# Optimization experiments

Hardware: AMD Instinct MI355X
Metric: run time of the kernel (lower is better)

Reference implementation:

```python
import jax, jax.numpy as jnp
import numpy as np

B, T, C = 2, 1024, 1024
H = 16
HD = C // H
S = 512   # short_term_memory_size
L = 1024  # sum(long_term_memory_size)
THETA = 10000.0


def setup_inputs() -> dict:
    key = jax.random.key(0)
    ks = jax.random.split(key, 7)
    return {
        "x": jax.random.normal(ks[0], (B, T, C), jnp.float32),
        "short_term_memory": jax.random.normal(ks[1], (B, S, C), jnp.float32),
        "long_q": jax.random.normal(ks[2], (B, L, H, HD), jnp.float32),
        "long_k": jax.random.normal(ks[3], (B, L, H, HD), jnp.float32),
        "long_v": jax.random.normal(ks[4], (B, L, H, HD), jnp.float32),
        "w_attn": jax.random.normal(ks[5], (C, 3 * C), jnp.float32) * 0.02,
        "w_proj": jax.random.normal(ks[6], (C, C), jnp.float32) * 0.02,
    }


def _rope_cos_sin(seq_len, dim, theta):
    # llama-style precompute_freqs_cis: freqs over even indices, angles = t * freq
    inv = 1.0 / (theta ** (jnp.arange(0, dim, 2, dtype=jnp.float32) / dim))
    t = jnp.arange(seq_len, dtype=jnp.float32)
    ang = jnp.outer(t, inv)  # [seq, dim//2]
    return jnp.cos(ang), jnp.sin(ang)


def _apply_rope(x, cos, sin):
    # x: [B, seq, H, hd] viewed as interleaved complex pairs (llama apply_rotary_emb)
    xr = x.reshape(*x.shape[:-1], HD // 2, 2)
    x0, x1 = xr[..., 0], xr[..., 1]
    c = cos[None, :, None, :]
    s = sin[None, :, None, :]
    o0 = x0 * c - x1 * s
    o1 = x0 * s + x1 * c
    return jnp.stack([o0, o1], axis=-1).reshape(x.shape)


def _memory_mask():
    # create_memory_mask: tril over M=L+S+T, rows [L, L+S) fully visible
    M = L + S + T
    m = np.tril(np.ones((M, M), dtype=np.float32))
    m[L:L + S, :] = 1.0
    return jnp.asarray(m)


_MASK = _memory_mask()


def reference(x, short_term_memory, long_q, long_k, long_v, w_attn, w_proj):
    # prepend short-term memory tokens, project qkv
    xcat = jnp.concatenate([short_term_memory, x], axis=1)          # [B, S+T, C]
    qkv = xcat @ w_attn                                             # [B, S+T, 3C]
    q, k, v = jnp.split(qkv, 3, axis=-1)
    q = q.reshape(B, S + T, H, HD)
    k = k.reshape(B, S + T, H, HD)
    v = v.reshape(B, S + T, H, HD)
    # in-place rotary on the last S+T positions (long-term part untouched)
    cos, sin = _rope_cos_sin(S + T, HD, THETA)
    q = _apply_rope(q, cos, sin)
    k = _apply_rope(k, cos, sin)
    # concat pre-rotated long-term memory in front
    q = jnp.concatenate([long_q, q], axis=1)                        # [B, M, H, hd]
    k = jnp.concatenate([long_k, k], axis=1)
    v = jnp.concatenate([long_v, v], axis=1)
    q, k, v = (t.transpose(0, 2, 1, 3) for t in (q, k, v))          # [B, H, M, hd]
    att = jnp.einsum('bhqd,bhkd->bhqk', q, k) * (1.0 / jnp.sqrt(jnp.float32(HD)))
    att = jnp.where(_MASK == 0, -jnp.inf, att)
    att = jax.nn.softmax(att, axis=-1)
    y = jnp.einsum('bhqk,bhkd->bhqd', att, v)                       # [B, H, M, hd]
    y = y.transpose(0, 2, 1, 3).reshape(B, L + S + T, C)
    y = y[:, -T:, :] @ w_proj                                       # [B, T, C]
    return y
```

## Files before the change

kernel.cpp:

```cpp
#include <hip/hip_runtime.h>
#include <math.h>

#define BB 2
#define TT 1024
#define CC 1024
#define HH 16
#define HD 64
#define SS 512
#define LL 1024
#define ST 1536
#define MM 2560
#define C3 3072

typedef __attribute__((ext_vector_type(8))) short short8;
typedef __attribute__((ext_vector_type(4))) short short4v;
typedef __attribute__((ext_vector_type(4))) float floatx4;

__device__ __forceinline__ unsigned short f2bf(float f) {
    union { float f; unsigned u; } v; v.f = f;
    unsigned r = v.u + 0x7fffu + ((v.u >> 16) & 1u);
    return (unsigned short)(r >> 16);
}
__device__ __forceinline__ float bf2f(short s) {
    union { unsigned u; float f; } v;
    v.u = ((unsigned)(unsigned short)s) << 16;
    return v.f;
}

__device__ __forceinline__ void gl_lds16(const short* g, short* l) {
    __builtin_amdgcn_global_load_lds(
        (const __attribute__((address_space(1))) void*)g,
        (__attribute__((address_space(3))) void*)l,
        16, 0, 0);
}

__global__ __launch_bounds__(256)
void prep_all(const float* __restrict__ x, const float* __restrict__ stm,
              const float* __restrict__ w_attn, const float* __restrict__ w_proj,
              const float* __restrict__ lk, const float* __restrict__ lv,
              short* __restrict__ Xb, short* __restrict__ WaT,
              short* __restrict__ WpT, short* __restrict__ Kg,
              short* __restrict__ Vt, float* __restrict__ tab)
{
    __shared__ __align__(16) char smem[9216];
    const int blk = blockIdx.x;
    const int t = threadIdx.x;

    if (blk < 3072) {
        const int idx = blk * 256 + t;
        const int rg  = idx >> 8;
        const int c   = (idx & 255) << 2;
        const int b   = rg >= ST;
        const int r   = rg - b * ST;
        const float* src = (r < SS) ? (stm + ((size_t)b * SS + r) * CC + c)
                                    : (x   + ((size_t)b * TT + (r - SS)) * CC + c);
        float4 v = *(const float4*)src;
        short4v o;
        o.x = (short)f2bf(v.x); o.y = (short)f2bf(v.y);
        o.z = (short)f2bf(v.z); o.w = (short)f2bf(v.w);
        *(short4v*)(Xb + (size_t)rg * CC + c) = o;
    } else if (blk < 7168) {
        const bool isA = blk < 6144;
        const int bx = isA ? (blk - 3072) : (blk - 6144);
        const int nblk = isA ? 96 : 32;
        const int Nd = isA ? C3 : CC;
        const float* W = isA ? w_attn : w_proj;
        short* WT = isA ? WaT : WpT;
        const int n0 = (bx % nblk) * 32, k0 = (bx / nblk) * 32;
        float (*Tl)[33] = (float(*)[33])smem;
        const int r = t >> 3, c4 = (t & 7) << 2;
        float4 v = *(const float4*)(W + (size_t)(k0 + r) * Nd + n0 + c4);
        Tl[r][c4 + 0] = v.x; Tl[r][c4 + 1] = v.y;
        Tl[r][c4 + 2] = v.z; Tl[r][c4 + 3] = v.w;
        __syncthreads();
        short4v o;
        o.x = (short)f2bf(Tl[c4 + 0][r]); o.y = (short)f2bf(Tl[c4 + 1][r]);
        o.z = (short)f2bf(Tl[c4 + 2][r]); o.w = (short)f2bf(Tl[c4 + 3][r]);
        *(short4v*)(WT + (size_t)(n0 + r) * CC + k0 + c4) = o;
    } else if (blk < 7360) {
        const int idx = (blk - 7168) * 256 + t;
        const int r = idx >> 5, e = idx & 31;
        const float inv = powf(10000.0f, -(float)e * (1.0f / 32.0f));
        float sn, cs;
        sincosf((float)r * inv, &sn, &cs);
        tab[idx * 2] = cs;
        tab[idx * 2 + 1] = sn;
    } else {
        const int bx = blk - 7360;
        const int bh = bx >> 4, j0 = (bx & 15) * 64;
        const int b = bh >> 4, h = bh & 15;
        short (*Tl)[72] = (short(*)[72])smem;
        const int jr = t >> 2, c16 = (t & 3) << 4;
        const size_t si = (((size_t)b * LL + j0 + jr) * HH + h) * HD + c16;
        short kk[16], vv[16];
        #pragma unroll
        for (int u = 0; u < 4; u++) {
            float4 kv = *(const float4*)(lk + si + 4 * u);
            float4 vf = *(const float4*)(lv + si + 4 * u);
            kk[4*u+0] = (short)f2bf(kv.x); kk[4*u+1] = (short)f2bf(kv.y);
            kk[4*u+2] = (short)f2bf(kv.z); kk[4*u+3] = (short)f2bf(kv.w);
            vv[4*u+0] = (short)f2bf(vf.x); vv[4*u+1] = (short)f2bf(vf.y);
            vv[4*u+2] = (short)f2bf(vf.z); vv[4*u+3] = (short)f2bf(vf.w);
        }
        short* kdst = Kg + ((size_t)bh * MM + j0 + jr) * HD + c16;
        *(short8*)kdst       = *(short8*)&kk[0];
        *(short8*)(kdst + 8) = *(short8*)&kk[8];
        #pragma unroll
        for (int u = 0; u < 16; u++) Tl[jr][c16 + u] = vv[u];
        __syncthreads();
        const int r = t >> 2, c = t & 3;
        short o0[8], o1[8];
        #pragma unroll
        for (int u = 0; u < 8; u++) {
            o0[u] = Tl[c * 16 + u][r];
            o1[u] = Tl[c * 16 + 8 + u][r];
        }
        short* vdst = Vt + ((size_t)bh * HD + r) * MM + j0 + c * 16;
        *(short8*)vdst       = *(short8*)&o0[0];
        *(short8*)(vdst + 8) = *(short8*)&o1[0];
    }
}

__global__ __launch_bounds__(256)
void qkv_gemm(const short* __restrict__ A, const short* __restrict__ Bt,
              const float* __restrict__ RT,
              short* __restrict__ Qo, short* __restrict__ Ko, short* __restrict__ Vo)
{
    __shared__ short As[128 * 32];
    __shared__ short Bs[128 * 32];
    __shared__ short Et[128 * 132];
    const int b = blockIdx.z;
    const int row0 = blockIdx.y * 128, col0 = blockIdx.x * 128;
    const int tid = threadIdx.x;
    const int w = tid >> 6, l = tid & 63, quad = l >> 4, cl = l & 15;
    const int wr = w >> 1, wc = w & 1;

    const int reg  = col0 >> 10;
    const bool hasQ = (row0 >= SS);
    if (reg == 0 && !hasQ) return;

    const int srow = (l >> 2);
    const int schunk = ((l & 3) - (srow >> 1)) & 3;
    const int arow = w * 32 + srow;
    const short* gA0 = A + ((size_t)b * ST + row0 + arow) * CC + schunk * 8;
    const short* gA1 = gA0 + (size_t)16 * CC;
    const short* gB0 = Bt + (size_t)(col0 + arow) * CC + schunk * 8;
    const short* gB1 = gB0 + (size_t)16 * CC;
    short* lA0 = &As[(w * 32) * 32 + l * 8];
    short* lA1 = &As[(w * 32 + 16) * 32 + l * 8];
    short* lB0 = &Bs[(w * 32) * 32 + l * 8];
    short* lB1 = &Bs[(w * 32 + 16) * 32 + l * 8];

    const int fs = (quad + (cl >> 1)) & 3;

    floatx4 acc[4][4];
    #pragma unroll
    for (int mi = 0; mi < 4; mi++)
        #pragma unroll
        for (int ni = 0; ni < 4; ni++) acc[mi][ni] = (floatx4){0.f, 0.f, 0.f, 0.f};

    for (int k0 = 0; k0 < CC; k0 += 32) {
        __syncthreads();
        gl_lds16(gA0 + k0, lA0);
        gl_lds16(gA1 + k0, lA1);
        gl_lds16(gB0 + k0, lB0);
        gl_lds16(gB1 + k0, lB1);
        __syncthreads();
        short8 af[4], bf[4];
        #pragma unroll
        for (int mi = 0; mi < 4; mi++)
            af[mi] = *(const short8*)&As[(wr * 64 + mi * 16 + cl) * 32 + fs * 8];
        #pragma unroll
        for (int ni = 0; ni < 4; ni++)
            bf[ni] = *(const short8*)&Bs[(wc * 64 + ni * 16 + cl) * 32 + fs * 8];
        #pragma unroll
        for (int mi = 0; mi < 4; mi++)
            #pragma unroll
            for (int ni = 0; ni < 4; ni++)
                acc[mi][ni] = __builtin_amdgcn_mfma_f32_16x16x32_bf16(
                    af[mi], bf[ni], acc[mi][ni], 0, 0, 0);
    }

    #pragma unroll
    for (int ni = 0; ni < 4; ni++) {
        const int c_local = wc * 64 + ni * 16 + cl;
        const int e = (c_local & 63) >> 1;
        #pragma unroll
        for (int mi = 0; mi < 4; mi++) {
            #pragma unroll
            for (int r = 0; r < 4; r++) {
                const int R_local = wr * 64 + mi * 16 + quad * 4 + r;
                const int R = row0 + R_local;
                float v = acc[mi][ni][r];
                if (reg < 2) {
                    const float2 tt = ((const float2*)RT)[R * 32 + e];
                    float po = __shfl_xor(v, 1);
                    float out = ((cl & 1) == 0) ? (v * tt.x - po * tt.y)
                                                : (po * tt.y + v * tt.x);
                    unsigned short bfv = f2bf(out);
                    int ob = __shfl_xor((int)bfv, 1);
                    if ((cl & 1) == 0) {
                        unsigned word = (unsigned)bfv | (((unsigned)ob & 0xffffu) << 16);
                        *(unsigned*)&Et[R_local * 132 + c_local] = word;
                    }
                } else {
                    Et[c_local * 132 + R_local] = (short)f2bf(v);
                }
            }
        }
    }
    __syncthreads();

    const int hh0 = (col0 & 1023) >> 6;
    if (reg < 2) {
        #pragma unroll
        for (int hf = 0; hf < 2; hf++) {
            const int hh = hh0 + hf;
            short* dstb = (reg == 0)
                ? Qo + (((size_t)b * HH + hh) * TT + (row0 - SS)) * HD
                : Ko + (((size_t)b * HH + hh) * MM + LL + row0) * HD;
            #pragma unroll
            for (int it = 0; it < 4; it++) {
                const int idx = it * 2048 + tid * 8;
                const int r = idx >> 6, d = idx & 63;
                short4v v0 = *(const short4v*)&Et[r * 132 + hf * 64 + d];
                short4v v1 = *(const short4v*)&Et[r * 132 + hf * 64 + d + 4];
                short8 vv;
                #pragma unroll
                for (int u = 0; u < 4; u++) { vv[u] = v0[u]; vv[u + 4] = v1[u]; }
                *(short8*)(dstb + idx) = vv;
            }
        }
    } else {
        #pragma unroll
        for (int it = 0; it < 8; it++) {
            const int idx = it * 2048 + tid * 8;
            const int c = idx >> 7, r0 = idx & 127;
            const int hh = hh0 + (c >> 6), d = c & 63;
            short4v v0 = *(const short4v*)&Et[c * 132 + r0];
            short4v v1 = *(const short4v*)&Et[c * 132 + r0 + 4];
            short8 vv;
            #pragma unroll
            for (int u = 0; u < 4; u++) { vv[u] = v0[u]; vv[u + 4] = v1[u]; }
            *(short8*)(Vo + (((size_t)b * HH + hh) * HD + d) * MM + LL + row0 + r0) = vv;
        }
    }
}

#define PSP 72
#define PSW (32 * PSP)
#define PS_OFF 16384
__global__ __launch_bounds__(256, 3)
void attn_mfma(const short* __restrict__ Qg, const short* __restrict__ Kg,
               const short* __restrict__ Vt, short* __restrict__ Op,
               float* __restrict__ Lp)
{
    __shared__ __align__(16) short L[25600];

    const int bh = blockIdx.x;
    const int q0 = (7 - blockIdx.y) * 128;
    const int piece = blockIdx.z;
    const int tid = threadIdx.x, w = tid >> 6, l = tid & 63;
    const int quad = l >> 4, cl = l & 15;

    short8 qa[2][2];
    #pragma unroll
    for (int g = 0; g < 2; g++) {
        const short* qptr = Qg + ((size_t)bh * TT + q0 + w * 32 + g * 16 + cl) * HD + quad * 8;
        qa[g][0] = *(const short8*)qptr;
        qa[g][1] = *(const short8*)(qptr + 32);
    }

    floatx4 o[2][4];
    float rs[2][4];
    #pragma unroll
    for (int g = 0; g < 2; g++)
        #pragma unroll
        for (int r = 0; r < 4; r++) {
            rs[g][r] = 0.f;
            o[g][r] = (floatx4){0.f, 0.f, 0.f, 0.f};
        }

    const int srow_lo = l >> 3;
    const int sslot  = l & 7;
    const int ch0 = (sslot - (srow_lo >> 1)) & 7;
    const int ch1 = (sslot - (4 + (srow_lo >> 1))) & 7;
    const int rowi0 = w * 16 + srow_lo;
    const int rowi1 = rowi0 + 8;
    const short* kgb = Kg + (size_t)bh * MM * HD;
    const short* vbase = Vt + (size_t)bh * HD * MM;

    const int fsA = (quad + (cl >> 1)) & 7;
    const int fsB = (quad + 4 + (cl >> 1)) & 7;
    const int psA = (quad + 2 * cl) & 7;
    const int psB = (quad + 4 + 2 * cl) & 7;

    const int ntiles = (LL + SS + q0) / 64 + 2;
    const int t_begin = piece * ntiles / 4;
    const int t_end   = (piece + 1) * ntiles / 4;
    const int t_tail  = ntiles - 2;

#define STAGE(tt, bb) do {                                                    \
    const int jj0 = (tt) * 64;                                                \
    short* lk_ = &L[((bb) << 13) + (w << 10)];                                \
    short* lv_ = lk_ + 4096;                                                  \
    gl_lds16(kgb + (size_t)(jj0 + rowi0) * HD + ch0 * 8, lk_);                \
    gl_lds16(kgb + (size_t)(jj0 + rowi1) * HD + ch1 * 8, lk_ + 512);          \
    gl_lds16(vbase + (size_t)rowi0 * MM + jj0 + ch0 * 8, lv_);                \
    gl_lds16(vbase + (size_t)rowi1 * MM + jj0 + ch1 * 8, lv_ + 512);          \
} while (0)

#define TILE(tt, kb_, TAILZONE) do {                                          \
    const int jj0 = (tt) * 64; (void)jj0;                                     \
    floatx4 s[2][4];                                                          \
    _Pragma("unroll")                                                         \
    for (int ks = 0; ks < 4; ks++) {                                          \
        const int krow = ks * 16 + cl;                                        \
        short8 kf0 = *(const short8*)&L[(kb_) + krow * 64 + fsA * 8];         \
        short8 kf1 = *(const short8*)&L[(kb_) + krow * 64 + fsB * 8];         \
        _Pragma("unroll")                                                     \
        for (int g = 0; g < 2; g++) {                                         \
            floatx4 z = (floatx4){0.f, 0.f, 0.f, 0.f};                        \
            z = __builtin_amdgcn_mfma_f32_16x16x32_bf16(qa[g][0], kf0, z, 0, 0, 0); \
            z = __builtin_amdgcn_mfma_f32_16x16x32_bf16(qa[g][1], kf1, z, 0, 0, 0); \
            s[g][ks] = z;                                                     \
        }                                                                     \
    }                                                                         \
    _Pragma("unroll")                                                         \
    for (int g = 0; g < 2; g++) {                                             \
        const int qgb = LL + SS + q0 + w * 32 + g * 16; (void)qgb;            \
        unsigned pw[4][4];                                                    \
        _Pragma("unroll")                                                     \
        for (int ks = 0; ks < 4; ks++) {                                      \
            _Pragma("unroll")                                                 \
            for (int r = 0; r < 4; r++) {                                     \
                float sv = s[g][ks][r] * 0.125f;                              \
                if (TAILZONE) {                                               \
                    if (jj0 + ks * 16 + cl > qgb + quad * 4 + r)              \
                        sv = -INFINITY;                                       \
                }                                                             \
                const float p = __expf(sv);                                   \
                rs[g][r] += p;                                                \
                const float po = __shfl_xor(p, 1);                            \
                unsigned w32;                                                 \
                asm("v_cvt_pk_bf16_f32 %0, %1, %2"                            \
                    : "=v"(w32) : "v"(p), "v"(po));                           \
                pw[ks][r] = w32;                                              \
            }                                                                 \
        }                                                                     \
        if ((cl & 1) == 0) {                                                  \
            _Pragma("unroll")                                                 \
            for (int ks = 0; ks < 4; ks++) {                                  \
                _Pragma("unroll")                                             \
                for (int r = 0; r < 4; r++) {                                 \
                    const int qrw = quad * 4 + r;                             \
                    const int slot = (ks * 2 + (cl >> 3) + 2 * qrw) & 7;      \
                    *(unsigned*)&L[PS_OFF + w * PSW + (g * 16 + qrw) * PSP    \
                                   + slot * 8 + (cl & 7)] = pw[ks][r];        \
                }                                                             \
            }                                                                 \
        }                                                                     \
    }                                                                         \
    __builtin_amdgcn_s_waitcnt(0xc07f);       \
    __builtin_amdgcn_wave_barrier();                                          \
    short8 pf[2][2];                                                          \
    _Pragma("unroll")                                                         \
    for (int g = 0; g < 2; g++) {                                             \
        pf[g][0] = *(const short8*)&L[PS_OFF + w * PSW + (g * 16 + cl) * PSP + psA * 8]; \
        pf[g][1] = *(const short8*)&L[PS_OFF + w * PSW + (g * 16 + cl) * PSP + psB * 8]; \
    }                                                                         \
    _Pragma("unroll")                                                         \
    for (int nt = 0; nt < 4; nt++) {                                          \
        const int drow = nt * 16 + cl;                                        \
        short8 vf0 = *(const short8*)&L[(kb_) + 4096 + drow * 64 + fsA * 8];  \
        short8 vf1 = *(const short8*)&L[(kb_) + 4096 + drow * 64 + fsB * 8];  \
        _Pragma("unroll")                                                     \
        for (int g = 0; g < 2; g++) {                                         \
            o[g][nt] = __builtin_amdgcn_mfma_f32_16x16x32_bf16(pf[g][0], vf0, o[g][nt], 0, 0, 0); \
            o[g][nt] = __builtin_amdgcn_mfma_f32_16x16x32_bf16(pf[g][1], vf1, o[g][nt], 0, 0, 0); \
        }                                                                     \
    }                                                                         \
} while (0)

    int cur = 0;
    if (t_begin < t_end) STAGE(t_begin, 0);
    for (int t = t_begin; t < t_end; t++) {
        const int nb = cur ^ 1;
        if (t + 1 < t_end) {
            STAGE(t + 1, nb);
            __builtin_amdgcn_s_waitcnt(0x0F74);
        } else {
            __builtin_amdgcn_s_waitcnt(0x0F70);
        }
        __builtin_amdgcn_s_barrier();
        __builtin_amdgcn_sched_barrier(0);
        const int kb = cur << 13;
        if (t < t_tail) { TILE(t, kb, 0); }
        else            { TILE(t, kb, 1); }
        __builtin_amdgcn_s_waitcnt(0xc07f);
        __builtin_amdgcn_sched_barrier(0);
        __builtin_amdgcn_s_barrier();
        cur = nb;
    }
#undef STAGE
#undef TILE

    #pragma unroll
    for (int g = 0; g < 2; g++)
        #pragma unroll
        for (int r = 0; r < 4; r++) {
            float t2 = rs[g][r];
            t2 += __shfl_xor(t2, 1);
            t2 += __shfl_xor(t2, 2);
            t2 += __shfl_xor(t2, 4);
            t2 += __shfl_xor(t2, 8);
            if (cl == 0)
                Lp[piece * 32768 + bh * 1024 + q0 + w * 32 + g * 16 + quad * 4 + r] = t2;
        }

    __syncthreads();
    #pragma unroll
    for (int g = 0; g < 2; g++)
        #pragma unroll
        for (int r = 0; r < 4; r++) {
            const int ql = w * 32 + g * 16 + quad * 4 + r;
            #pragma unroll
            for (int nt = 0; nt < 4; nt++)
                L[ql * 68 + nt * 16 + cl] = (short)f2bf(o[g][nt][r]);
        }
    __syncthreads();
    short* ob = Op + ((size_t)(piece * 32 + bh) * 1024 + q0) * 64;
    #pragma unroll
    for (int it = 0; it < 4; it++) {
        const int idx = it * 2048 + tid * 8;
        const int q = idx >> 6, d = idx & 63;
        short4v v0 = *(const short4v*)&L[q * 68 + d];
        short4v v1 = *(const short4v*)&L[q * 68 + d + 4];
        short8 vv;
        #pragma unroll
        for (int u = 0; u < 4; u++) { vv[u] = v0[u]; vv[u + 4] = v1[u]; }
        *(short8*)(ob + idx) = vv;
    }
}

__global__ __launch_bounds__(256)
void attn_combine(const short* __restrict__ Op, const float* __restrict__ Lp,
                  short* __restrict__ Yatt)
{
    const int idx = blockIdx.x * 256 + threadIdx.x;
    const int row = idx >> 3;
    const int seg = (idx & 7) << 3;
    const float lsum = Lp[row] + Lp[32768 + row] + Lp[65536 + row] + Lp[98304 + row];
    const float inv = 1.0f / lsum;
    float acc[8] = {0.f, 0.f, 0.f, 0.f, 0.f, 0.f, 0.f, 0.f};
    #pragma unroll
    for (int p = 0; p < 4; p++) {
        short8 v = *(const short8*)(Op + ((size_t)(p * 32768) + row) * 64 + seg);
        #pragma unroll
        for (int u = 0; u < 8; u++) acc[u] += bf2f(v[u]);
    }
    short8 o8;
    #pragma unroll
    for (int u = 0; u < 8; u++) o8[u] = (short)f2bf(acc[u] * inv);
    const int bh = row >> 10, q = row & 1023;
    const int b = bh >> 4, h = bh & 15;
    *(short8*)(Yatt + ((size_t)b * TT + q) * CC + h * 64 + seg) = o8;
}

__global__ __launch_bounds__(256)
void proj_gemm(const short* __restrict__ A, const short* __restrict__ Bt,
               float* __restrict__ Co)
{
    __shared__ short As[64 * 32];
    __shared__ short Bs[64 * 32];
    const int row0 = blockIdx.y * 64, col0 = blockIdx.x * 64;
    const int tid = threadIdx.x;
    const int w = tid >> 6, l = tid & 63, quad = l >> 4, cl = l & 15;
    const int wr = w >> 1, wc = w & 1;

    const int srow = tid >> 2;
    const int schunk = ((tid & 3) - ((srow & 15) >> 1)) & 3;
    const short* gA = A + (size_t)(row0 + srow) * CC + schunk * 8;
    const short* gB = Bt + (size_t)(col0 + srow) * CC + schunk * 8;
    short* lA = &As[tid * 8];
    short* lB = &Bs[tid * 8];

    const int fs = (quad + (cl >> 1)) & 3;

    floatx4 acc[2][2];
    #pragma unroll
    for (int mi = 0; mi < 2; mi++)
        #pragma unroll
        for (int ni = 0; ni < 2; ni++) acc[mi][ni] = (floatx4){0.f, 0.f, 0.f, 0.f};

    for (int k0 = 0; k0 < CC; k0 += 32) {
        __syncthreads();
        gl_lds16(gA + k0, lA);
        gl_lds16(gB + k0, lB);
        __syncthreads();
        short8 af[2], bf[2];
        #pragma unroll
        for (int mi = 0; mi < 2; mi++)
            af[mi] = *(const short8*)&As[(wr * 32 + mi * 16 + cl) * 32 + fs * 8];
        #pragma unroll
        for (int ni = 0; ni < 2; ni++)
            bf[ni] = *(const short8*)&Bs[(wc * 32 + ni * 16 + cl) * 32 + fs * 8];
        #pragma unroll
        for (int mi = 0; mi < 2; mi++)
            #pragma unroll
            for (int ni = 0; ni < 2; ni++)
                acc[mi][ni] = __builtin_amdgcn_mfma_f32_16x16x32_bf16(
                    af[mi], bf[ni], acc[mi][ni], 0, 0, 0);
    }
    #pragma unroll
    for (int mi = 0; mi < 2; mi++)
        #pragma unroll
        for (int ni = 0; ni < 2; ni++)
            #pragma unroll
            for (int r = 0; r < 4; r++)
                Co[(size_t)(row0 + wr * 32 + mi * 16 + quad * 4 + r) * CC
                   + col0 + wc * 32 + ni * 16 + cl] = acc[mi][ni][r];
}

extern "C" void kernel_launch(void* const* d_in, const int* in_sizes, int n_in,
                              void* d_out, int out_size, void* d_ws, size_t ws_size,
                              hipStream_t stream)
{
    (void)in_sizes; (void)n_in; (void)out_size; (void)ws_size;
    const float* x      = (const float*)d_in[0];
    const float* stm    = (const float*)d_in[1];
    const float* long_k = (const float*)d_in[3];
    const float* long_v = (const float*)d_in[4];
    const float* w_attn = (const float*)d_in[5];
    const float* w_proj = (const float*)d_in[6];
    float* out = (float*)d_out;

    short* Xb   = (short*)d_ws;
    short* WaT  = Xb   + (size_t)3145728;
    short* WpT  = WaT  + (size_t)3145728;
    short* Qb   = WpT  + (size_t)1048576;
    short* Kb   = Qb   + (size_t)2097152;
    short* Vtr  = Kb   + (size_t)5242880;
    short* Yb   = Vtr  + (size_t)5242880;
    float* RTab = (float*)(Yb + (size_t)2097152);
    short* Opart = (short*)(RTab + 98304);
    float* Lpart = (float*)(Opart + (size_t)8388608);

    prep_all<<<7872, 256, 0, stream>>>(x, stm, w_attn, w_proj, long_k, long_v,
                                       Xb, WaT, WpT, Kb, Vtr, RTab);

    qkv_gemm<<<dim3(24, 12, 2), 256, 0, stream>>>(Xb, WaT, RTab, Qb, Kb, Vtr);

    attn_mfma<<<dim3(32, 8, 4), 256, 0, stream>>>(Qb, Kb, Vtr, Opart, Lpart);
    attn_combine<<<1024, 256, 0, stream>>>(Opart, Lpart, Yb);

    proj_gemm<<<dim3(16, 32), 256, 0, stream>>>(Yb, WpT, out);
}
```

Before: 227.9 us.

## Single-buffer K/V staging in attention to raise occupancy to four blocks

The attention kernel no longer double-buffers K/V tiles in LDS. Each iteration now loads one K/V tile into a single buffer between two __syncthreads, instead of prefetching the next tile while computing the current one. This shrinks LDS per block from 25600 to 17408 shorts and raises the launch-bounds target from 3 to 4 blocks per CU. The cost is that global-to-LDS load latency is no longer overlapped within a block, so the kernel now relies on extra concurrent blocks to hide it.

New measurement: 216.6 us. 1.05x faster.

```diff
diff --git a/kernel.cpp b/kernel.cpp
--- a/kernel.cpp
+++ b/kernel.cpp
@@ -249,13 +249,14 @@
 
 #define PSP 72
 #define PSW (32 * PSP)
-#define PS_OFF 16384
-__global__ __launch_bounds__(256, 3)
+#define VS_OFF 4096
+#define PS_OFF 8192
+__global__ __launch_bounds__(256, 4)
 void attn_mfma(const short* __restrict__ Qg, const short* __restrict__ Kg,
                const short* __restrict__ Vt, short* __restrict__ Op,
                float* __restrict__ Lp)
 {
-    __shared__ __align__(16) short L[25600];
+    __shared__ __align__(16) short L[17408];
 
     const int bh = blockIdx.x;
     const int q0 = (7 - blockIdx.y) * 128;
@@ -286,9 +287,13 @@
     const int ch0 = (sslot - (srow_lo >> 1)) & 7;
     const int ch1 = (sslot - (4 + (srow_lo >> 1))) & 7;
     const int rowi0 = w * 16 + srow_lo;
-    const int rowi1 = rowi0 + 8;
+    const int rowi1 = w * 16 + 8 + srow_lo;
     const short* kgb = Kg + (size_t)bh * MM * HD;
     const short* vbase = Vt + (size_t)bh * HD * MM;
+    short* ldsK0 = &L[(w * 16) * 64];
+    short* ldsK1 = &L[(w * 16 + 8) * 64];
+    short* ldsV0 = &L[VS_OFF + (w * 16) * 64];
+    short* ldsV1 = &L[VS_OFF + (w * 16 + 8) * 64];
 
     const int fsA = (quad + (cl >> 1)) & 7;
     const int fsB = (quad + 4 + (cl >> 1)) & 7;
@@ -300,24 +305,14 @@
     const int t_end   = (piece + 1) * ntiles / 4;
     const int t_tail  = ntiles - 2;
 
-#define STAGE(tt, bb) do {                                                    \
-    const int jj0 = (tt) * 64;                                                \
-    short* lk_ = &L[((bb) << 13) + (w << 10)];                                \
-    short* lv_ = lk_ + 4096;                                                  \
-    gl_lds16(kgb + (size_t)(jj0 + rowi0) * HD + ch0 * 8, lk_);                \
-    gl_lds16(kgb + (size_t)(jj0 + rowi1) * HD + ch1 * 8, lk_ + 512);          \
-    gl_lds16(vbase + (size_t)rowi0 * MM + jj0 + ch0 * 8, lv_);                \
-    gl_lds16(vbase + (size_t)rowi1 * MM + jj0 + ch1 * 8, lv_ + 512);          \
-} while (0)
-
-#define TILE(tt, kb_, TAILZONE) do {                                          \
+#define TILE(tt, TAILZONE) do {                                               \
     const int jj0 = (tt) * 64; (void)jj0;                                     \
     floatx4 s[2][4];                                                          \
     _Pragma("unroll")                                                         \
     for (int ks = 0; ks < 4; ks++) {                                          \
         const int krow = ks * 16 + cl;                                        \
-        short8 kf0 = *(const short8*)&L[(kb_) + krow * 64 + fsA * 8];         \
-        short8 kf1 = *(const short8*)&L[(kb_) + krow * 64 + fsB * 8];         \
+        short8 kf0 = *(const short8*)&L[krow * 64 + fsA * 8];                 \
+        short8 kf1 = *(const short8*)&L[krow * 64 + fsB * 8];                 \
         _Pragma("unroll")                                                     \
         for (int g = 0; g < 2; g++) {                                         \
             floatx4 z = (floatx4){0.f, 0.f, 0.f, 0.f};                        \
@@ -372,8 +367,8 @@
     _Pragma("unroll")                                                         \
     for (int nt = 0; nt < 4; nt++) {                                          \
         const int drow = nt * 16 + cl;                                        \
-        short8 vf0 = *(const short8*)&L[(kb_) + 4096 + drow * 64 + fsA * 8];  \
-        short8 vf1 = *(const short8*)&L[(kb_) + 4096 + drow * 64 + fsB * 8];  \
+        short8 vf0 = *(const short8*)&L[VS_OFF + drow * 64 + fsA * 8];        \
+        short8 vf1 = *(const short8*)&L[VS_OFF + drow * 64 + fsB * 8];        \
         _Pragma("unroll")                                                     \
         for (int g = 0; g < 2; g++) {                                         \
             o[g][nt] = __builtin_amdgcn_mfma_f32_16x16x32_bf16(pf[g][0], vf0, o[g][nt], 0, 0, 0); \
@@ -382,27 +377,17 @@
     }                                                                         \
 } while (0)
 
-    int cur = 0;
-    if (t_begin < t_end) STAGE(t_begin, 0);
     for (int t = t_begin; t < t_end; t++) {
-        const int nb = cur ^ 1;
-        if (t + 1 < t_end) {
-            STAGE(t + 1, nb);
-            __builtin_amdgcn_s_waitcnt(0x0F74);
-        } else {
-            __builtin_amdgcn_s_waitcnt(0x0F70);
-        }
-        __builtin_amdgcn_s_barrier();
-        __builtin_amdgcn_sched_barrier(0);
-        const int kb = cur << 13;
-        if (t < t_tail) { TILE(t, kb, 0); }
-        else            { TILE(t, kb, 1); }
-        __builtin_amdgcn_s_waitcnt(0xc07f);
-        __builtin_amdgcn_sched_barrier(0);
-        __builtin_amdgcn_s_barrier();
-        cur = nb;
-    }
-#undef STAGE
+        const int j0 = t * 64;
+        __syncthreads();
+        gl_lds16(kgb + (size_t)(j0 + rowi0) * HD + ch0 * 8, ldsK0);
+        gl_lds16(kgb + (size_t)(j0 + rowi1) * HD + ch1 * 8, ldsK1);
+        gl_lds16(vbase + (size_t)rowi0 * MM + j0 + ch0 * 8, ldsV0);
+        gl_lds16(vbase + (size_t)rowi1 * MM + j0 + ch1 * 8, ldsV1);
+        __syncthreads();
+        if (t < t_tail) { TILE(t, 0); }
+        else            { TILE(t, 1); }
+    }
 #undef TILE
 
     #pragma unroll
```
